# Performance work log

Measured on AMD Instinct MI355X. Metric: run time of the kernel, lower is better.

The kernel has to match this reference:

```python
import jax, jax.numpy as jnp
import numpy as np

N_NODES = 50000


def gcn_conv(x, edge_index, W, b):
    """PyG GCNConv: add self-loops, sym-normalize, out = A_hat @ (x W) + b."""
    src, dst = edge_index[0], edge_index[1]
    n = x.shape[0]
    h = x @ W  # [N, out]
    # degree with self-loops (all edge weights = 1)
    deg = jax.ops.segment_sum(jnp.ones_like(dst, dtype=x.dtype), dst, num_segments=n) + 1.0
    dinv = jax.lax.rsqrt(deg)  # deg >= 1 so safe
    norm = dinv[src] * dinv[dst]  # [E]
    msgs = h[src] * norm[:, None]  # gather + scale
    agg = jax.ops.segment_sum(msgs, dst, num_segments=n)  # scatter-add
    agg = agg + h * (dinv * dinv)[:, None]  # self-loop term: norm_ii = dinv_i^2
    return agg + b


def setup_inputs() -> dict:
    key = jax.random.key(0)
    k_x, k_e, k_w1, k_w2 = jax.random.split(key, 4)
    in_ch, hid, out_ch = 256, 128, 128
    x = jax.random.normal(k_x, (N_NODES, in_ch), dtype=jnp.float32)
    edge_index = jax.random.randint(k_e, (2, 1_600_000), 0, N_NODES, dtype=jnp.int32)
    # Glorot-style init like PyG GCNConv
    W1 = jax.random.normal(k_w1, (in_ch, hid), dtype=jnp.float32) * (1.0 / np.sqrt(in_ch))
    b1 = jnp.zeros((hid,), dtype=jnp.float32)
    W2 = jax.random.normal(k_w2, (hid, out_ch), dtype=jnp.float32) * (1.0 / np.sqrt(hid))
    b2 = jnp.zeros((out_ch,), dtype=jnp.float32)
    return {"x": x, "edge_index": edge_index, "W1": W1, "b1": b1, "W2": W2, "b2": b2}


def reference(x, edge_index, W1, b1, W2, b2):
    # layer 1: GCNConv -> ReLU (dropout is identity in eval mode)
    h = jax.nn.relu(gcn_conv(x, edge_index, W1, b1))
    # layer 2: GCNConv -> ReLU
    out = jax.nn.relu(gcn_conv(h, edge_index, W2, b2))
    return out
```

## Files before the change

kernel.cpp:

```cpp
#include <hip/hip_runtime.h>
#include <cstdint>
#include <cstddef>


#define ELL_STRIDE 64
#define BCAP 8192
#define OVF_CAP 1024
#define PART_T 2048

typedef __attribute__((ext_vector_type(8))) short bf16x8;
typedef __attribute__((ext_vector_type(4))) float floatx4;

__device__ __forceinline__ unsigned short f2bf(float f) {
  unsigned int u = __float_as_uint(f);
  unsigned int r = (u + 0x7fffu + ((u >> 16) & 1u)) >> 16;
  return (unsigned short)r;
}
__device__ __forceinline__ float2 bfpair(unsigned int p) {
  float2 r;
  r.x = __uint_as_float(p << 16);
  r.y = __uint_as_float(p & 0xffff0000u);
  return r;
}

__global__ __launch_bounds__(256) void k_cvt_w(const float* __restrict__ W1,
                                               const float* __restrict__ W2,
                                               unsigned short* __restrict__ WT1,
                                               unsigned short* __restrict__ WT2,
                                               int* __restrict__ cursor,
                                               int* __restrict__ ovf_cnt,
                                               int NB) {
  int i = blockIdx.x * 256 + threadIdx.x;
  if (i < NB) cursor[i] = 0;
  if (i == NB) *ovf_cnt = 0;
  if (i < 128 * 256) {
    int n = i >> 8, k = i & 255;
    WT1[i] = f2bf(W1[k * 128 + n]);
  } else if (i < 128 * 256 + 128 * 128) {
    int j = i - 128 * 256;
    int n = j >> 7, k = j & 127;
    WT2[j] = f2bf(W2[k * 128 + n]);
  }
}

__global__ __launch_bounds__(256) void k_part(const int* __restrict__ src,
                                              const int* __restrict__ dst,
                                              int* __restrict__ cursor,
                                              unsigned int* __restrict__ part,
                                              int* __restrict__ ovf_cnt,
                                              int* __restrict__ ovf,
                                              int E, int NB) {
  __shared__ unsigned int stage1[PART_T];
  __shared__ unsigned int stage2[PART_T];
  __shared__ int hist[512];
  __shared__ int base_g[512];
  __shared__ int base_l[512];
  __shared__ int cl[512];
  __shared__ int sc[256];
  const int tid = threadIdx.x;
  const int e0 = blockIdx.x * PART_T;
  int valid = E - e0; if (valid > PART_T) valid = PART_T;

  hist[tid] = 0; hist[tid + 256] = 0;
  cl[tid] = 0; cl[tid + 256] = 0;
  __syncthreads();
  for (int i = tid; i < valid; i += 256) {
    int e = e0 + i;
    unsigned int v = (unsigned int)(src[e] & 0xffff) | ((unsigned int)dst[e] << 16);
    stage1[i] = v;
    atomicAdd(&hist[(v >> 16) >> 7], 1);
  }
  __syncthreads();
  for (int b = tid; b < NB; b += 256) base_g[b] = atomicAdd(&cursor[b], hist[b]);
  int h0 = hist[2 * tid], h1 = hist[2 * tid + 1];
  int pv = h0 + h1;
  sc[tid] = pv;
  __syncthreads();
  #pragma unroll
  for (int off = 1; off < 256; off <<= 1) {
    int t = (tid >= off) ? sc[tid - off] : 0;
    __syncthreads();
    sc[tid] += t;
    __syncthreads();
  }
  int excl = sc[tid] - pv;
  base_l[2 * tid] = excl;
  base_l[2 * tid + 1] = excl + h0;
  __syncthreads();
  for (int i = tid; i < valid; i += 256) {
    unsigned int v = stage1[i];
    int b = (v >> 16) >> 7;
    int pos = base_l[b] + atomicAdd(&cl[b], 1);
    stage2[pos] = v;
  }
  __syncthreads();
  for (int i = tid; i < valid; i += 256) {
    unsigned int v = stage2[i];
    int b = (v >> 16) >> 7;
    int g = base_g[b] + (i - base_l[b]);
    if (g < BCAP) {
      part[(size_t)b * BCAP + g] = v;
    } else {
      int p = atomicAdd(ovf_cnt, 1);
      if (p < OVF_CAP) { ovf[2 * p] = (int)(v & 0xffffu); ovf[2 * p + 1] = (int)(v >> 16); }
    }
  }
}

__global__ __launch_bounds__(256) void k_fill2(const unsigned int* __restrict__ part,
                                               const int* __restrict__ cursor,
                                               unsigned short* __restrict__ col,
                                               int* __restrict__ cnt,
                                               float* __restrict__ dinv,
                                               int* __restrict__ ovf_cnt,
                                               int* __restrict__ ovf, int N) {
  __shared__ unsigned short slab[128 * ELL_STRIDE];
  __shared__ int cl[128];
  const int tid = threadIdx.x;
  const int b = blockIdx.x;
  if (tid < 128) cl[tid] = 0;
  __syncthreads();
  int count = cursor[b]; if (count > BCAP) count = BCAP;
  const unsigned int* p = part + (size_t)b * BCAP;
  for (int i = tid; i < count; i += 256) {
    unsigned int v = p[i];
    int row = (v >> 16) & 127;
    int k = atomicAdd(&cl[row], 1);
    if (k < ELL_STRIDE) {
      slab[row * ELL_STRIDE + k] = (unsigned short)(v & 0xffffu);
    } else {
      int q = atomicAdd(ovf_cnt, 1);
      if (q < OVF_CAP) { ovf[2 * q] = (int)(v & 0xffffu); ovf[2 * q + 1] = (int)(v >> 16); }
    }
  }
  __syncthreads();
  uint4* d4 = (uint4*)(col + (size_t)b * 128 * ELL_STRIDE);
  const uint4* s4 = (const uint4*)slab;
  #pragma unroll
  for (int i = 0; i < (128 * ELL_STRIDE * 2) / (16 * 256); ++i)
    d4[i * 256 + tid] = s4[i * 256 + tid];
  if (tid < 128) {
    int node = b * 128 + tid;
    if (node < N) {
      int c = cl[tid];
      cnt[node] = c;
      dinv[node] = rsqrtf((float)c + 1.0f);
    }
  }
}

template <int K, bool AF32>
__global__ __launch_bounds__(512) void k_gemm_mfma(const void* __restrict__ Xv,
                                                   const unsigned short* __restrict__ WT,
                                                   const float* __restrict__ dinv,
                                                   unsigned short* __restrict__ hb,
                                                   int M) {
  constexpr int KP = K + 8;
  __shared__ unsigned short Bs[128 * KP];
  const int tid = threadIdx.x;
  const int wave = tid >> 6, lane = tid & 63;
  const int q = lane >> 4, m = lane & 15;
  const int row0 = blockIdx.x * 128 + wave * 16;
  const bool active = row0 < M;
  const int arow = row0 + m;

  for (int c = tid; c < 128 * (K / 8); c += 512) {
    int r = c / (K / 8), ko = (c % (K / 8)) * 8;
    *(uint4*)(Bs + r * KP + ko) = *(const uint4*)(WT + (size_t)r * K + ko);
  }

  bf16x8 af[K / 32];
  if (active) {
    #pragma unroll
    for (int ks = 0; ks < K / 32; ++ks) {
      const int k0 = ks * 32 + q * 8;
      if (AF32) {
        const float* X = (const float*)Xv;
        float4 a0 = *(const float4*)(X + (size_t)arow * K + k0);
        float4 a1 = *(const float4*)(X + (size_t)arow * K + k0 + 4);
        af[ks] = (bf16x8){(short)f2bf(a0.x), (short)f2bf(a0.y),
                          (short)f2bf(a0.z), (short)f2bf(a0.w),
                          (short)f2bf(a1.x), (short)f2bf(a1.y),
                          (short)f2bf(a1.z), (short)f2bf(a1.w)};
      } else {
        af[ks] = *(const bf16x8*)((const unsigned short*)Xv +
                                  (size_t)arow * K + k0);
      }
    }
  }
  __syncthreads();
  if (!active) return;

  floatx4 acc[8];
  #pragma unroll
  for (int nt = 0; nt < 8; ++nt) acc[nt] = (floatx4){0.f, 0.f, 0.f, 0.f};
  #pragma unroll
  for (int ks = 0; ks < K / 32; ++ks) {
    const int k0 = ks * 32 + q * 8;
    #pragma unroll
    for (int nt = 0; nt < 8; ++nt) {
      bf16x8 bf = *(const bf16x8*)(Bs + (nt * 16 + m) * KP + k0);
      acc[nt] = __builtin_amdgcn_mfma_f32_16x16x32_bf16(af[ks], bf, acc[nt], 0, 0, 0);
    }
  }
  #pragma unroll
  for (int r = 0; r < 4; ++r) {
    int grow = row0 + q * 4 + r;
    float di = dinv[grow];
    #pragma unroll
    for (int nt = 0; nt < 8; ++nt)
      hb[(size_t)(nt >> 1) * M * 32 + (size_t)grow * 32 + (nt & 1) * 16 + m] =
          f2bf(acc[nt][r] * di);
  }
}

template <bool BF16OUT>
__global__ __launch_bounds__(256) void k_agg(const unsigned int* __restrict__ hb,
                                             const int* __restrict__ cnt,
                                             const unsigned short* __restrict__ col,
                                             const float* __restrict__ dinv,
                                             const int* __restrict__ ovf_cnt,
                                             const int* __restrict__ ovf,
                                             const float* __restrict__ bias,
                                             void* __restrict__ outv, int n) {
  __shared__ unsigned short cols[32][ELL_STRIDE];
  const int tid = threadIdx.x;
  const int chunk = blockIdx.x & 3;
  const int nd0 = (blockIdx.x >> 2) * 32;
  {
    int s = tid * 16;
    int node = nd0 + (s >> 6);
    uint4 v0 = make_uint4(0, 0, 0, 0), v1 = v0;
    if (node < n) {
      v0 = *(const uint4*)(col + (size_t)node * ELL_STRIDE + (s & 63));
      v1 = *(const uint4*)(col + (size_t)node * ELL_STRIDE + (s & 63) + 8);
    }
    *(uint4*)&cols[s >> 6][s & 63] = v0;
    *(uint4*)&cols[s >> 6][(s & 63) + 8] = v1;
  }
  __syncthreads();
  const int nodeL = tid >> 3;
  const int d = nd0 + nodeL;
  const int w = tid & 7;
  if (d >= n) return;
  const uint2* slab = (const uint2*)hb + (size_t)chunk * n * 8;
  const unsigned short* lc = cols[nodeL];

  uint2 sv = slab[(size_t)d * 8 + w];
  float2 s0 = bfpair(sv.x), s1 = bfpair(sv.y);
  float a0 = s0.x, a1 = s0.y, a2 = s1.x, a3 = s1.y;

  int m = cnt[d]; if (m > ELL_STRIDE) m = ELL_STRIDE;
  int k = 0;
#define GATH(P)                                                   \
  {                                                               \
    float2 _x = bfpair((P).x), _y = bfpair((P).y);                \
    a0 += _x.x; a1 += _x.y; a2 += _y.x; a3 += _y.y;               \
  }
  for (; k + 16 <= m; k += 16) {
    ushort4 ca = *(const ushort4*)(lc + k);
    ushort4 cb = *(const ushort4*)(lc + k + 4);
    ushort4 cc = *(const ushort4*)(lc + k + 8);
    ushort4 cd = *(const ushort4*)(lc + k + 12);
    uint2 p0 = slab[(size_t)ca.x * 8 + w];
    uint2 p1 = slab[(size_t)ca.y * 8 + w];
    uint2 p2 = slab[(size_t)ca.z * 8 + w];
    uint2 p3 = slab[(size_t)ca.w * 8 + w];
    uint2 p4 = slab[(size_t)cb.x * 8 + w];
    uint2 p5 = slab[(size_t)cb.y * 8 + w];
    uint2 p6 = slab[(size_t)cb.z * 8 + w];
    uint2 p7 = slab[(size_t)cb.w * 8 + w];
    uint2 p8 = slab[(size_t)cc.x * 8 + w];
    uint2 p9 = slab[(size_t)cc.y * 8 + w];
    uint2 pa = slab[(size_t)cc.z * 8 + w];
    uint2 pb = slab[(size_t)cc.w * 8 + w];
    uint2 pc = slab[(size_t)cd.x * 8 + w];
    uint2 pd = slab[(size_t)cd.y * 8 + w];
    uint2 pe = slab[(size_t)cd.z * 8 + w];
    uint2 pf = slab[(size_t)cd.w * 8 + w];
    GATH(p0) GATH(p1) GATH(p2) GATH(p3) GATH(p4) GATH(p5) GATH(p6) GATH(p7)
    GATH(p8) GATH(p9) GATH(pa) GATH(pb) GATH(pc) GATH(pd) GATH(pe) GATH(pf)
  }
  for (; k + 8 <= m; k += 8) {
    ushort4 ca = *(const ushort4*)(lc + k);
    ushort4 cb = *(const ushort4*)(lc + k + 4);
    uint2 p0 = slab[(size_t)ca.x * 8 + w];
    uint2 p1 = slab[(size_t)ca.y * 8 + w];
    uint2 p2 = slab[(size_t)ca.z * 8 + w];
    uint2 p3 = slab[(size_t)ca.w * 8 + w];
    uint2 p4 = slab[(size_t)cb.x * 8 + w];
    uint2 p5 = slab[(size_t)cb.y * 8 + w];
    uint2 p6 = slab[(size_t)cb.z * 8 + w];
    uint2 p7 = slab[(size_t)cb.w * 8 + w];
    GATH(p0) GATH(p1) GATH(p2) GATH(p3) GATH(p4) GATH(p5) GATH(p6) GATH(p7)
  }
  for (; k < m; ++k) {
    uint2 p = slab[(size_t)lc[k] * 8 + w];
    GATH(p)
  }
  int V = *ovf_cnt; if (V > OVF_CAP) V = OVF_CAP;
  for (int j = 0; j < V; ++j) {
    if (ovf[2 * j + 1] == d) {
      uint2 p = slab[(size_t)ovf[2 * j] * 8 + w];
      GATH(p)
    }
  }
#undef GATH
  float di = dinv[d];
  float4 bv = *(const float4*)(bias + chunk * 32 + w * 4);
  float r0 = fmaxf(di * a0 + bv.x, 0.f);
  float r1 = fmaxf(di * a1 + bv.y, 0.f);
  float r2 = fmaxf(di * a2 + bv.z, 0.f);
  float r3 = fmaxf(di * a3 + bv.w, 0.f);
  if (BF16OUT) {
    uint2 pk;
    pk.x = (unsigned int)f2bf(r0) | ((unsigned int)f2bf(r1) << 16);
    pk.y = (unsigned int)f2bf(r2) | ((unsigned int)f2bf(r3) << 16);
    ((uint2*)outv)[(size_t)d * 32 + chunk * 8 + w] = pk;
  } else {
    *(float4*)((float*)outv + (size_t)d * 128 + chunk * 32 + w * 4) =
        make_float4(r0, r1, r2, r3);
  }
}

extern "C" void kernel_launch(void* const* d_in, const int* in_sizes, int n_in,
                              void* d_out, int out_size, void* d_ws, size_t ws_size,
                              hipStream_t stream) {
  const float* x  = (const float*)d_in[0];
  const int*   ei = (const int*)d_in[1];
  const float* W1 = (const float*)d_in[2];
  const float* b1 = (const float*)d_in[3];
  const float* W2 = (const float*)d_in[4];
  const float* b2 = (const float*)d_in[5];
  float* out = (float*)d_out;

  const int IN_CH = 256;
  const int N = in_sizes[0] / IN_CH;
  const int E = in_sizes[1] / 2;
  const int NB = (N + 127) >> 7;

  const int* src = ei;
  const int* dst = ei + E;

  char* ws = (char*)d_ws;
  size_t off = 0;
  auto carve = [&](size_t bytes) {
    void* p = ws + off;
    off += (bytes + 255) & ~(size_t)255;
    return p;
  };
  int*            cursor  = (int*)carve((size_t)NB * 4);
  int*            ovf_cnt = (int*)carve(4);
  int*            ovf     = (int*)carve((size_t)OVF_CAP * 2 * 4);
  int*            cnt     = (int*)carve((size_t)N * 4);
  float*          dinv    = (float*)carve((size_t)N * 4);
  unsigned short* col     = (unsigned short*)carve((size_t)N * ELL_STRIDE * 2);
  unsigned short* hb      = (unsigned short*)carve((size_t)N * 128 * 2);
  unsigned short* WT1     = (unsigned short*)carve(128 * 256 * 2);
  unsigned short* WT2     = (unsigned short*)carve(128 * 128 * 2);
  char*           unionp  = (char*)carve((size_t)NB * BCAP * 4);
  unsigned int*   part    = (unsigned int*)unionp;
  unsigned short* aggbuf  = (unsigned short*)unionp;

  k_cvt_w<<<(128 * 256 + 128 * 128 + 255) / 256, 256, 0, stream>>>(
      W1, W2, WT1, WT2, cursor, ovf_cnt, NB);
  k_part <<<(E + PART_T - 1) / PART_T, 256, 0, stream>>>(src, dst, cursor, part,
                                                         ovf_cnt, ovf, E, NB);
  k_fill2<<<NB, 256, 0, stream>>>(part, cursor, col, cnt, dinv, ovf_cnt, ovf, N);

  int gblocks = (N + 127) / 128;
  int ablocks = 4 * ((N + 31) / 32);
  k_gemm_mfma<256, true ><<<gblocks, 512, 0, stream>>>(x, WT1, dinv, hb, N);
  k_agg<true ><<<ablocks, 256, 0, stream>>>((const unsigned int*)hb, cnt, col, dinv,
                                            ovf_cnt, ovf, b1, aggbuf, N);
  k_gemm_mfma<128, false><<<gblocks, 512, 0, stream>>>(aggbuf, WT2, dinv, hb, N);
  k_agg<false><<<ablocks, 256, 0, stream>>>((const unsigned int*)hb, cnt, col, dinv,
                                            ovf_cnt, ovf, b2, out, N);
}
```

Baseline: 253.1 us.

## Widen aggregation gathers to 16-byte loads with zero-row padded ELL lists

Each node in the aggregation is now handled by 4 lanes loading uint4 (8 bf16) instead of 8 lanes loading uint2, and each block covers 64 nodes. ELL slots are pre-filled with a sentinel index N that points to an all-zero padding row appended to each feature chunk. This lets the inner loop run in branch-free steps of 8 up to the per-wave maximum degree, with no remainder loops. The aim is fewer memory instructions and less divergence. The cost is wasted gathers of the zero row when degrees vary within a wave, and one extra row per chunk of storage.

Measured after the change: 235.6 us. -6.9%, faster.

```diff
diff --git a/kernel.cpp b/kernel.cpp
--- a/kernel.cpp
+++ b/kernel.cpp
@@ -29,10 +29,15 @@
                                                unsigned short* __restrict__ WT2,
                                                int* __restrict__ cursor,
                                                int* __restrict__ ovf_cnt,
-                                               int NB) {
+                                               unsigned short* __restrict__ hb,
+                                               int N, int NB) {
   int i = blockIdx.x * 256 + threadIdx.x;
   if (i < NB) cursor[i] = 0;
   if (i == NB) *ovf_cnt = 0;
+  if (i < 128) {
+    int chunk = i >> 5, j = i & 31;
+    hb[(size_t)chunk * (N + 1) * 32 + (size_t)N * 32 + j] = 0;
+  }
   if (i < 128 * 256) {
     int n = i >> 8, k = i & 255;
     WT1[i] = f2bf(W1[k * 128 + n]);
@@ -119,6 +124,13 @@
   const int tid = threadIdx.x;
   const int b = blockIdx.x;
   if (tid < 128) cl[tid] = 0;
+  {
+    unsigned int dpk = ((unsigned int)N << 16) | (unsigned int)N;
+    unsigned int* s32 = (unsigned int*)slab;
+    #pragma unroll
+    for (int i = 0; i < (128 * ELL_STRIDE / 2) / 256; ++i)
+      s32[i * 256 + tid] = dpk;
+  }
   __syncthreads();
   int count = cursor[b]; if (count > BCAP) count = BCAP;
   const unsigned int* p = part + (size_t)b * BCAP;
@@ -209,13 +221,13 @@
     float di = dinv[grow];
     #pragma unroll
     for (int nt = 0; nt < 8; ++nt)
-      hb[(size_t)(nt >> 1) * M * 32 + (size_t)grow * 32 + (nt & 1) * 16 + m] =
+      hb[(size_t)(nt >> 1) * (M + 1) * 32 + (size_t)grow * 32 + (nt & 1) * 16 + m] =
           f2bf(acc[nt][r] * di);
   }
 }
 
 template <bool BF16OUT>
-__global__ __launch_bounds__(256) void k_agg(const unsigned int* __restrict__ hb,
+__global__ __launch_bounds__(256) void k_agg(const uint4* __restrict__ hb4,
                                              const int* __restrict__ cnt,
                                              const unsigned short* __restrict__ col,
                                              const float* __restrict__ dinv,
@@ -223,103 +235,98 @@
                                              const int* __restrict__ ovf,
                                              const float* __restrict__ bias,
                                              void* __restrict__ outv, int n) {
-  __shared__ unsigned short cols[32][ELL_STRIDE];
+  __shared__ unsigned short cols[64][72];
   const int tid = threadIdx.x;
   const int chunk = blockIdx.x & 3;
-  const int nd0 = (blockIdx.x >> 2) * 32;
+  const int nd0 = (blockIdx.x >> 2) * 64;
   {
+    unsigned int dpk = ((unsigned int)n << 16) | (unsigned int)n;
     int s = tid * 16;
-    int node = nd0 + (s >> 6);
-    uint4 v0 = make_uint4(0, 0, 0, 0), v1 = v0;
-    if (node < n) {
-      v0 = *(const uint4*)(col + (size_t)node * ELL_STRIDE + (s & 63));
-      v1 = *(const uint4*)(col + (size_t)node * ELL_STRIDE + (s & 63) + 8);
-    }
-    *(uint4*)&cols[s >> 6][s & 63] = v0;
-    *(uint4*)&cols[s >> 6][(s & 63) + 8] = v1;
-  }
-  __syncthreads();
-  const int nodeL = tid >> 3;
+    int node = s >> 6, off = s & 63;
+    uint4 v0 = make_uint4(dpk, dpk, dpk, dpk), v1 = v0;
+    if (nd0 + node < n) {
+      v0 = *(const uint4*)(col + (size_t)(nd0 + node) * ELL_STRIDE + off);
+      v1 = *(const uint4*)(col + (size_t)(nd0 + node) * ELL_STRIDE + off + 8);
+    }
+    *(uint4*)&cols[node][off] = v0;
+    *(uint4*)&cols[node][off + 8] = v1;
+  }
+  __syncthreads();
+  const int wave = tid >> 6, lane = tid & 63;
+  const int nodeL = wave * 16 + (lane >> 2);
+  const int q = lane & 3;
   const int d = nd0 + nodeL;
-  const int w = tid & 7;
-  if (d >= n) return;
-  const uint2* slab = (const uint2*)hb + (size_t)chunk * n * 8;
+  const bool valid = d < n;
+  const uint4* slab = hb4 + (size_t)chunk * (n + 1) * 4;
   const unsigned short* lc = cols[nodeL];
 
-  uint2 sv = slab[(size_t)d * 8 + w];
-  float2 s0 = bfpair(sv.x), s1 = bfpair(sv.y);
-  float a0 = s0.x, a1 = s0.y, a2 = s1.x, a3 = s1.y;
-
-  int m = cnt[d]; if (m > ELL_STRIDE) m = ELL_STRIDE;
-  int k = 0;
-#define GATH(P)                                                   \
-  {                                                               \
-    float2 _x = bfpair((P).x), _y = bfpair((P).y);                \
-    a0 += _x.x; a1 += _x.y; a2 += _y.x; a3 += _y.y;               \
-  }
-  for (; k + 16 <= m; k += 16) {
+  float a0 = 0.f, a1 = 0.f, a2 = 0.f, a3 = 0.f;
+  float a4 = 0.f, a5 = 0.f, a6 = 0.f, a7 = 0.f;
+#define ADDP(P)                                                            \
+  {                                                                        \
+    float2 x0 = bfpair((P).x), x1 = bfpair((P).y);                         \
+    float2 x2 = bfpair((P).z), x3 = bfpair((P).w);                         \
+    a0 += x0.x; a1 += x0.y; a2 += x1.x; a3 += x1.y;                        \
+    a4 += x2.x; a5 += x2.y; a6 += x3.x; a7 += x3.y;                        \
+  }
+  if (valid) {
+    uint4 p = slab[(size_t)d * 4 + q];
+    ADDP(p)
+  }
+  int m = valid ? cnt[d] : 0; if (m > ELL_STRIDE) m = ELL_STRIDE;
+  int mmax = m;
+  #pragma unroll
+  for (int s = 4; s < 64; s <<= 1) {
+    int o = __shfl_xor(mmax, s);
+    mmax = o > mmax ? o : mmax;
+  }
+  for (int k = 0; k < mmax; k += 8) {
     ushort4 ca = *(const ushort4*)(lc + k);
     ushort4 cb = *(const ushort4*)(lc + k + 4);
-    ushort4 cc = *(const ushort4*)(lc + k + 8);
-    ushort4 cd = *(const ushort4*)(lc + k + 12);
-    uint2 p0 = slab[(size_t)ca.x * 8 + w];
-    uint2 p1 = slab[(size_t)ca.y * 8 + w];
-    uint2 p2 = slab[(size_t)ca.z * 8 + w];
-    uint2 p3 = slab[(size_t)ca.w * 8 + w];
-    uint2 p4 = slab[(size_t)cb.x * 8 + w];
-    uint2 p5 = slab[(size_t)cb.y * 8 + w];
-    uint2 p6 = slab[(size_t)cb.z * 8 + w];
-    uint2 p7 = slab[(size_t)cb.w * 8 + w];
-    uint2 p8 = slab[(size_t)cc.x * 8 + w];
-    uint2 p9 = slab[(size_t)cc.y * 8 + w];
-    uint2 pa = slab[(size_t)cc.z * 8 + w];
-    uint2 pb = slab[(size_t)cc.w * 8 + w];
-    uint2 pc = slab[(size_t)cd.x * 8 + w];
-    uint2 pd = slab[(size_t)cd.y * 8 + w];
-    uint2 pe = slab[(size_t)cd.z * 8 + w];
-    uint2 pf = slab[(size_t)cd.w * 8 + w];
-    GATH(p0) GATH(p1) GATH(p2) GATH(p3) GATH(p4) GATH(p5) GATH(p6) GATH(p7)
-    GATH(p8) GATH(p9) GATH(pa) GATH(pb) GATH(pc) GATH(pd) GATH(pe) GATH(pf)
-  }
-  for (; k + 8 <= m; k += 8) {
-    ushort4 ca = *(const ushort4*)(lc + k);
-    ushort4 cb = *(const ushort4*)(lc + k + 4);
-    uint2 p0 = slab[(size_t)ca.x * 8 + w];
-    uint2 p1 = slab[(size_t)ca.y * 8 + w];
-    uint2 p2 = slab[(size_t)ca.z * 8 + w];
-    uint2 p3 = slab[(size_t)ca.w * 8 + w];
-    uint2 p4 = slab[(size_t)cb.x * 8 + w];
-    uint2 p5 = slab[(size_t)cb.y * 8 + w];
-    uint2 p6 = slab[(size_t)cb.z * 8 + w];
-    uint2 p7 = slab[(size_t)cb.w * 8 + w];
-    GATH(p0) GATH(p1) GATH(p2) GATH(p3) GATH(p4) GATH(p5) GATH(p6) GATH(p7)
-  }
-  for (; k < m; ++k) {
-    uint2 p = slab[(size_t)lc[k] * 8 + w];
-    GATH(p)
-  }
-  int V = *ovf_cnt; if (V > OVF_CAP) V = OVF_CAP;
-  for (int j = 0; j < V; ++j) {
-    if (ovf[2 * j + 1] == d) {
-      uint2 p = slab[(size_t)ovf[2 * j] * 8 + w];
-      GATH(p)
-    }
-  }
-#undef GATH
+    uint4 p0 = slab[(size_t)ca.x * 4 + q];
+    uint4 p1 = slab[(size_t)ca.y * 4 + q];
+    uint4 p2 = slab[(size_t)ca.z * 4 + q];
+    uint4 p3 = slab[(size_t)ca.w * 4 + q];
+    uint4 p4 = slab[(size_t)cb.x * 4 + q];
+    uint4 p5 = slab[(size_t)cb.y * 4 + q];
+    uint4 p6 = slab[(size_t)cb.z * 4 + q];
+    uint4 p7 = slab[(size_t)cb.w * 4 + q];
+    ADDP(p0) ADDP(p1) ADDP(p2) ADDP(p3)
+    ADDP(p4) ADDP(p5) ADDP(p6) ADDP(p7)
+  }
+  if (valid) {
+    int V = *ovf_cnt; if (V > OVF_CAP) V = OVF_CAP;
+    for (int j = 0; j < V; ++j) {
+      if (ovf[2 * j + 1] == d) {
+        uint4 p = slab[(size_t)ovf[2 * j] * 4 + q];
+        ADDP(p)
+      }
+    }
+  }
+#undef ADDP
+  if (!valid) return;
   float di = dinv[d];
-  float4 bv = *(const float4*)(bias + chunk * 32 + w * 4);
-  float r0 = fmaxf(di * a0 + bv.x, 0.f);
-  float r1 = fmaxf(di * a1 + bv.y, 0.f);
-  float r2 = fmaxf(di * a2 + bv.z, 0.f);
-  float r3 = fmaxf(di * a3 + bv.w, 0.f);
+  float4 b0 = *(const float4*)(bias + chunk * 32 + q * 8);
+  float4 b1 = *(const float4*)(bias + chunk * 32 + q * 8 + 4);
+  float r0 = fmaxf(di * a0 + b0.x, 0.f);
+  float r1 = fmaxf(di * a1 + b0.y, 0.f);
+  float r2 = fmaxf(di * a2 + b0.z, 0.f);
+  float r3 = fmaxf(di * a3 + b0.w, 0.f);
+  float r4 = fmaxf(di * a4 + b1.x, 0.f);
+  float r5 = fmaxf(di * a5 + b1.y, 0.f);
+  float r6 = fmaxf(di * a6 + b1.z, 0.f);
+  float r7 = fmaxf(di * a7 + b1.w, 0.f);
   if (BF16OUT) {
-    uint2 pk;
+    uint4 pk;
     pk.x = (unsigned int)f2bf(r0) | ((unsigned int)f2bf(r1) << 16);
     pk.y = (unsigned int)f2bf(r2) | ((unsigned int)f2bf(r3) << 16);
-    ((uint2*)outv)[(size_t)d * 32 + chunk * 8 + w] = pk;
+    pk.z = (unsigned int)f2bf(r4) | ((unsigned int)f2bf(r5) << 16);
+    pk.w = (unsigned int)f2bf(r6) | ((unsigned int)f2bf(r7) << 16);
+    ((uint4*)outv)[(size_t)d * 16 + chunk * 4 + q] = pk;
   } else {
-    *(float4*)((float*)outv + (size_t)d * 128 + chunk * 32 + w * 4) =
-        make_float4(r0, r1, r2, r3);
+    float* o = (float*)outv + (size_t)d * 128 + chunk * 32 + q * 8;
+    *(float4*)o = make_float4(r0, r1, r2, r3);
+    *(float4*)(o + 4) = make_float4(r4, r5, r6, r7);
   }
 }
 
@@ -355,7 +362,7 @@
   int*            cnt     = (int*)carve((size_t)N * 4);
   float*          dinv    = (float*)carve((size_t)N * 4);
   unsigned short* col     = (unsigned short*)carve((size_t)N * ELL_STRIDE * 2);
-  unsigned short* hb      = (unsigned short*)carve((size_t)N * 128 * 2);
+  unsigned short* hb      = (unsigned short*)carve((size_t)(N + 1) * 256);
   unsigned short* WT1     = (unsigned short*)carve(128 * 256 * 2);
   unsigned short* WT2     = (unsigned short*)carve(128 * 128 * 2);
   char*           unionp  = (char*)carve((size_t)NB * BCAP * 4);
@@ -363,17 +370,17 @@
   unsigned short* aggbuf  = (unsigned short*)unionp;
 
   k_cvt_w<<<(128 * 256 + 128 * 128 + 255) / 256, 256, 0, stream>>>(
-      W1, W2, WT1, WT2, cursor, ovf_cnt, NB);
+      W1, W2, WT1, WT2, cursor, ovf_cnt, hb, N, NB);
   k_part <<<(E + PART_T - 1) / PART_T, 256, 0, stream>>>(src, dst, cursor, part,
                                                          ovf_cnt, ovf, E, NB);
   k_fill2<<<NB, 256, 0, stream>>>(part, cursor, col, cnt, dinv, ovf_cnt, ovf, N);
 
   int gblocks = (N + 127) / 128;
-  int ablocks = 4 * ((N + 31) / 32);
+  int ablocks = 4 * ((N + 63) / 64);
   k_gemm_mfma<256, true ><<<gblocks, 512, 0, stream>>>(x, WT1, dinv, hb, N);
-  k_agg<true ><<<ablocks, 256, 0, stream>>>((const unsigned int*)hb, cnt, col, dinv,
+  k_agg<true ><<<ablocks, 256, 0, stream>>>((const uint4*)hb, cnt, col, dinv,
                                             ovf_cnt, ovf, b1, aggbuf, N);
   k_gemm_mfma<128, false><<<gblocks, 512, 0, stream>>>(aggbuf, WT2, dinv, hb, N);
-  k_agg<false><<<ablocks, 256, 0, stream>>>((const unsigned int*)hb, cnt, col, dinv,
+  k_agg<false><<<ablocks, 256, 0, stream>>>((const uint4*)hb, cnt, col, dinv,
                                             ovf_cnt, ovf, b2, out, N);
 }
```
